# Performance work log

Measured on AMD Instinct MI355X. Metric: run time of the kernel, lower is better.

The kernel has to match this reference:

```python
import jax, jax.numpy as jnp
import numpy as np
import math

B, S, D, H = 64, 512, 768, 12
HS = D // H  # head size = 64


def setup_inputs() -> dict:
    key = jax.random.key(0)
    ks = jax.random.split(key, 8)
    scale = 1.0 / math.sqrt(D)
    return {
        "from_tensor": jax.random.normal(ks[0], (B, S, D), jnp.float32),
        "to_tensor": jax.random.normal(ks[1], (B, S, D), jnp.float32),
        "Wq": jax.random.normal(ks[2], (D, D), jnp.float32) * scale,
        "bq": jax.random.normal(ks[3], (D,), jnp.float32) * 0.02,
        "Wk": jax.random.normal(ks[4], (D, D), jnp.float32) * scale,
        "bk": jax.random.normal(ks[5], (D,), jnp.float32) * 0.02,
        "Wv": jax.random.normal(ks[6], (D, D), jnp.float32) * scale,
        "bv": jax.random.normal(ks[7], (D,), jnp.float32) * 0.02,
    }


def _split_heads(x):
    # [B, S, D] -> [B, H, S, HS]
    return x.reshape(B, S, H, HS).transpose(0, 2, 1, 3)


def reference(from_tensor, to_tensor, Wq, bq, Wk, bk, Wv, bv):
    q = _split_heads(from_tensor @ Wq + bq)
    k = _split_heads(to_tensor @ Wk + bk)
    v = _split_heads(to_tensor @ Wv + bv)
    scores = jnp.einsum("bhqd,bhkd->bhqk", q, k) / math.sqrt(HS)
    probs = jax.nn.softmax(scores, axis=-1)
    out = jnp.einsum("bhqk,bhkd->bhqd", probs, v)
    return out.transpose(0, 2, 1, 3).reshape(B, S, D)
```

## Files before the change

kernel.cpp:

```cpp
#include <hip/hip_runtime.h>
#include <hip/hip_bf16.h>

#define GAS __attribute__((address_space(1)))
#define LAS __attribute__((address_space(3)))

typedef __attribute__((ext_vector_type(8))) short   bf16x8;
typedef __attribute__((ext_vector_type(4))) float   f32x4;
typedef __attribute__((ext_vector_type(16))) float  f32x16;
typedef __attribute__((ext_vector_type(4))) float   f4;
typedef __attribute__((ext_vector_type(8))) short   s8v;
typedef __attribute__((ext_vector_type(2))) unsigned int u32x2;
typedef __attribute__((ext_vector_type(4))) unsigned int u32x4;

#define NB  64
#define NS  512
#define ND  768
#define NH  12
#define NHS 64
#define NM  (NB*NS)
#define NBH (NB*NH)

#define QSCALE 0.18033688011112042f

__device__ __forceinline__ unsigned short f2bf(float x){
  unsigned int u = __float_as_uint(x);
  u += 0x7fffu + ((u >> 16) & 1u);
  return (unsigned short)(u >> 16);
}

__device__ __forceinline__ f32x4 mfma16(bf16x8 a, bf16x8 b, f32x4 c){
  return __builtin_amdgcn_mfma_f32_16x16x32_bf16(a, b, c, 0, 0, 0);
}

__device__ __forceinline__ f32x16 mfma32(bf16x8 a, bf16x8 b, f32x16 c){
  return __builtin_amdgcn_mfma_f32_32x32x16_bf16(a, b, c, 0, 0, 0);
}

__device__ __forceinline__ unsigned int cvtpk(float lo, float hi){
  unsigned int r;
  asm("v_cvt_pk_bf16_f32 %0, %1, %2" : "=v"(r) : "v"(lo), "v"(hi));
  return r;
}

__device__ __forceinline__ bf16x8 u2b(u32x4 u){
  union { u32x4 a; bf16x8 b; } c; c.a = u; return c.b;
}

__global__ void cvt_w(const float* __restrict__ Wq, const float* __restrict__ Wk,
                      const float* __restrict__ Wv, short* __restrict__ Wt){
  int i = blockIdx.x * 256 + threadIdx.x;
  int mat = i / (ND*ND);
  int rem = i - mat * (ND*ND);
  int k = rem / ND;
  int n = rem - k * ND;
  const float* W = (mat == 0) ? Wq : (mat == 1 ? Wk : Wv);
  Wt[(long)mat*ND*ND + (long)n*ND + k] = (short)f2bf(W[rem]);
}

__global__ __launch_bounds__(512, 2)
void qkv_gemm(const float* __restrict__ from_t, const float* __restrict__ to_t,
              const short* __restrict__ Wt,
              const float* __restrict__ bq, const float* __restrict__ bk,
              const float* __restrict__ bv,
              short* __restrict__ Qw, short* __restrict__ Kw, short* __restrict__ Vtw){
  __shared__ short smem[65536];

  int bid = blockIdx.x;
  int wg  = (bid & 7) * 144 + (bid >> 3);
  int mat = wg / 384;
  int r   = wg - mat * 384;
  int mt  = r / 3;
  int nt  = r - mt * 3;

  const float* Af = (mat == 0) ? from_t : to_t;
  const short* Wp = Wt + (long)mat * ND * ND;

  int t_ = threadIdx.x, wv = t_ >> 6, l = t_ & 63, g = l >> 4, c = l & 15;
  int wm = wv >> 2, wn = wv & 3;
  int m0 = mt * 256, n0 = nt * 256;

  f4 areg[4];

  auto stageA_load = [&](int kt2){
    #pragma unroll
    for (int j = 0; j < 2; ++j){
      int idx = j * 512 + t_;
      int row = idx >> 2, slot = idx & 3;
      const float* gp = Af + (long)(m0 + row) * ND + kt2 * 32 + slot * 8;
      areg[j * 2]     = *(const f4*)(gp);
      areg[j * 2 + 1] = *(const f4*)(gp + 4);
    }
  };
  auto stageA_write = [&](int kt2){
    short* base = smem + (kt2 & 3) * 8192;
    #pragma unroll
    for (int j = 0; j < 2; ++j){
      int idx = j * 512 + t_;
      int row = idx >> 2, slot = idx & 3;
      int sw = slot ^ ((row >> 1) & 3);
      u32x4 pk;
      pk[0] = cvtpk(areg[j * 2][0],     areg[j * 2][1]);
      pk[1] = cvtpk(areg[j * 2][2],     areg[j * 2][3]);
      pk[2] = cvtpk(areg[j * 2 + 1][0], areg[j * 2 + 1][1]);
      pk[3] = cvtpk(areg[j * 2 + 1][2], areg[j * 2 + 1][3]);
      *(bf16x8*)(base + row * 32 + sw * 8) = u2b(pk);
    }
  };
  auto stageB = [&](int kt2){
    short* base = smem + 32768 + (kt2 & 3) * 8192;
    #pragma unroll
    for (int j = 0; j < 2; ++j){
      int idx = j * 512 + t_;
      int row = idx >> 2, slot = idx & 3;
      const short* gp = Wp + (long)(n0 + row) * ND + kt2 * 32 + ((slot ^ ((row >> 1) & 3)) << 3);
      __builtin_amdgcn_global_load_lds((const GAS unsigned int*)gp,
                                       (LAS unsigned int*)(base + idx * 8), 16, 0, 0);
    }
  };

  f32x4 zero = {0.f, 0.f, 0.f, 0.f};
  f32x4 acc[8][4];
  #pragma unroll
  for (int i = 0; i < 8; ++i)
    #pragma unroll
    for (int j = 0; j < 4; ++j) acc[i][j] = zero;

  stageB(0);
  stageA_load(0);
  stageA_write(0);
  stageA_load(1);
  stageA_write(1);
  stageA_load(2);
  stageB(1); stageB(2);
  asm volatile("s_waitcnt vmcnt(8)" ::: "memory");
  asm volatile("s_waitcnt lgkmcnt(0)" ::: "memory");
  __builtin_amdgcn_s_barrier();

  bf16x8 bfr[4];
  for (int kt = 0; kt < 24; ++kt){
    int sl = kt & 3;
    const short* Asl = smem + sl * 8192;
    const short* Bsl = smem + 32768 + sl * 8192;

    bf16x8 af[4];
    #pragma unroll
    for (int i = 0; i < 4; ++i){
      int row = wm * 128 + i * 16 + c;
      af[i] = *(const bf16x8*)(Asl + row * 32 + ((g ^ ((row >> 1) & 3)) << 3));
    }
    #pragma unroll
    for (int ns = 0; ns < 4; ++ns){
      int row = wn * 64 + ns * 16 + c;
      bfr[ns] = *(const bf16x8*)(Bsl + row * 32 + ((g ^ ((row >> 1) & 3)) << 3));
    }
    if (kt < 22) stageA_write(kt + 2);
    if (kt < 21) stageA_load(kt + 3);
    __builtin_amdgcn_s_barrier();
    asm volatile("s_waitcnt lgkmcnt(0)" ::: "memory");
    __builtin_amdgcn_sched_barrier(0);
    __builtin_amdgcn_s_setprio(1);
    #pragma unroll
    for (int i = 0; i < 4; ++i)
      #pragma unroll
      for (int ns = 0; ns < 4; ++ns)
        acc[i][ns] = mfma16(af[i], bfr[ns], acc[i][ns]);
    __builtin_amdgcn_s_setprio(0);
    __builtin_amdgcn_s_barrier();

    #pragma unroll
    for (int i = 0; i < 4; ++i){
      int row = wm * 128 + (4 + i) * 16 + c;
      af[i] = *(const bf16x8*)(Asl + row * 32 + ((g ^ ((row >> 1) & 3)) << 3));
    }
    if (kt < 21) stageB(kt + 3);
    __builtin_amdgcn_s_barrier();
    asm volatile("s_waitcnt lgkmcnt(0)" ::: "memory");
    __builtin_amdgcn_sched_barrier(0);
    __builtin_amdgcn_s_setprio(1);
    #pragma unroll
    for (int i = 0; i < 4; ++i)
      #pragma unroll
      for (int ns = 0; ns < 4; ++ns)
        acc[4 + i][ns] = mfma16(af[i], bfr[ns], acc[4 + i][ns]);
    __builtin_amdgcn_s_setprio(0);
    if (kt <= 20)      asm volatile("s_waitcnt vmcnt(8)" ::: "memory");
    else if (kt == 21) asm volatile("s_waitcnt vmcnt(2)" ::: "memory");
    else if (kt == 22) asm volatile("s_waitcnt vmcnt(0)" ::: "memory");
    __builtin_amdgcn_s_barrier();
  }

  int n0g = n0 + wn * 64;
  const float* bias = (mat == 0) ? bq : (mat == 1 ? bk : bv);
  float bb[4];
  #pragma unroll
  for (int ns = 0; ns < 4; ++ns) bb[ns] = bias[n0g + ns * 16 + c];
  short* chunk = smem + wv * 4096;
  int hq = n0g >> 6;

  if (mat < 2){
    short* O = (mat == 0) ? Qw : Kw;
    float scl = (mat == 0) ? QSCALE : 1.0f;
    #pragma unroll
    for (int sp = 0; sp < 2; ++sp){
      #pragma unroll
      for (int msl = 0; msl < 4; ++msl){
        #pragma unroll
        for (int ns = 0; ns < 4; ++ns){
          int col = ns * 16 + c;
          #pragma unroll
          for (int i = 0; i < 4; ++i){
            int row = msl * 16 + g * 4 + i;
            chunk[row * 64 + (((col >> 3) ^ (row & 7)) << 3) + (col & 7)] =
                (short)f2bf((acc[sp * 4 + msl][ns][i] + bb[ns]) * scl);
          }
        }
      }
      asm volatile("s_waitcnt lgkmcnt(0)" ::: "memory");
      __builtin_amdgcn_sched_barrier(0);
      #pragma unroll
      for (int rr = 0; rr < 8; ++rr){
        int row = rr * 8 + (l >> 3);
        int slot = l & 7;
        bf16x8 v = *(const bf16x8*)(chunk + row * 64 + ((slot ^ (row & 7)) << 3));
        int m = m0 + wm * 128 + sp * 64 + row;
        int b = m >> 9, s2 = m & 511;
        *(bf16x8*)(O + (((long)(b * NH + hq) * NS + s2) << 6) + slot * 8) = v;
      }
      if (sp == 0){ asm volatile("s_waitcnt lgkmcnt(0)" ::: "memory"); }
    }
  } else {
    #pragma unroll
    for (int sp = 0; sp < 2; ++sp){
      #pragma unroll
      for (int msl = 0; msl < 4; ++msl){
        #pragma unroll
        for (int ns = 0; ns < 4; ++ns){
          int hs = ns * 16 + c;
          #pragma unroll
          for (int i = 0; i < 4; ++i){
            int col = msl * 16 + g * 4 + i;
            chunk[hs * 64 + (((col >> 3) ^ (hs & 7)) << 3) + (col & 7)] =
                (short)f2bf(acc[sp * 4 + msl][ns][i] + bb[ns]);
          }
        }
      }
      asm volatile("s_waitcnt lgkmcnt(0)" ::: "memory");
      __builtin_amdgcn_sched_barrier(0);
      int mbase = m0 + wm * 128 + sp * 64;
      int b = mbase >> 9, s0 = mbase & 511;
      #pragma unroll
      for (int rr = 0; rr < 8; ++rr){
        int hs = rr * 8 + (l >> 3);
        int slot = l & 7;
        bf16x8 v = *(const bf16x8*)(chunk + hs * 64 + ((slot ^ (hs & 7)) << 3));
        *(bf16x8*)(Vtw + (long)((b * NH + hq) * 64 + hs) * NS + s0 + slot * 8) = v;
      }
      if (sp == 0){ asm volatile("s_waitcnt lgkmcnt(0)" ::: "memory"); }
    }
  }
}

__global__ __launch_bounds__(512, 1)
void attn_kernel(const short* __restrict__ Qw, const short* __restrict__ Kw,
                 const short* __restrict__ Vtw, float* __restrict__ out){
  extern __shared__ char smem[];
  short* Ks = (short*)smem;
  short* Vs = (short*)(smem + 65536);

  int bh = blockIdx.x;
  int t = threadIdx.x, wv = t >> 6, l = t & 63;
  int lam = l & 31, hi = l >> 5;
  int r7 = lam & 7;

  const short* Kb = Kw  + (long)bh * NS * NHS;
  const short* Vb = Vtw + (long)bh * NS * NHS;

  #pragma unroll
  for (int it = 0; it < 8; ++it){
    int chunk = it * 8 + wv;
    {
      int idx = chunk * 64 + l;
      int row = idx >> 3, slot = idx & 7;
      const short* gk = Kb + row * 64 + ((slot ^ (row & 7)) * 8);
      __builtin_amdgcn_global_load_lds((const GAS unsigned int*)gk,
                                       (LAS unsigned int*)(Ks + chunk * 512), 16, 0, 0);
    }
    {
      int row = chunk, slot = l;
      const short* gv = Vb + (long)row * NS + (((slot & 56) | ((slot & 7) ^ (row & 7))) * 8);
      __builtin_amdgcn_global_load_lds((const GAS unsigned int*)gv,
                                       (LAS unsigned int*)(Vs + chunk * 512), 16, 0, 0);
    }
  }
  __syncthreads();

  int b = bh / NH, h = bh - b * NH;
  float* outb = out + (long)b * NS * ND + (long)h * 64;

  for (int qt = 0; qt < 2; ++qt){
    int q0 = wv * 64 + qt * 32;
    const short* Qb = Qw + (((long)bh * NS + q0 + lam) << 6) + hi * 8;
    bf16x8 qf[4];
    #pragma unroll
    for (int dk = 0; dk < 4; ++dk) qf[dk] = *(const bf16x8*)(Qb + dk * 16);

    f32x16 o0, o1;
    #pragma unroll
    for (int j = 0; j < 16; ++j){ o0[j] = 0.f; o1[j] = 0.f; }
    float m_run = -1e30f, lsum = 0.f;

    #pragma unroll
    for (int ch = 0; ch < 16; ++ch){
      f32x16 s;
      #pragma unroll
      for (int j = 0; j < 16; ++j) s[j] = 0.f;
      const char* kbase = (const char*)Ks + (ch * 32 + lam) * 128;
      #pragma unroll
      for (int dk = 0; dk < 4; ++dk){
        bf16x8 kf = *(const bf16x8*)(kbase + (((hi + 2 * dk) ^ r7) << 4));
        s = mfma32(kf, qf[dk], s);
      }

      float t8[8], t4[4];
      #pragma unroll
      for (int j = 0; j < 8; ++j) t8[j] = fmaxf(s[j], s[j + 8]);
      #pragma unroll
      for (int j = 0; j < 4; ++j) t4[j] = fmaxf(t8[j], t8[j + 4]);
      float m1 = fmaxf(fmaxf(t4[0], t4[1]), fmaxf(t4[2], t4[3]));
      float pmax = fmaxf(m1, __shfl_xor(m1, 32));
      if (__any(pmax > m_run + 8.0f)){
        float mnew = fmaxf(m_run, pmax);
        float cf = exp2f(m_run - mnew);
        lsum *= cf;
        #pragma unroll
        for (int j = 0; j < 16; ++j){ o0[j] *= cf; o1[j] *= cf; }
        m_run = mnew;
      }
      float p[16];
      #pragma unroll
      for (int j = 0; j < 16; ++j) p[j] = exp2f(s[j] - m_run);
      float a8[8], a4[4];
      #pragma unroll
      for (int j = 0; j < 8; ++j) a8[j] = p[j] + p[j + 8];
      #pragma unroll
      for (int j = 0; j < 4; ++j) a4[j] = a8[j] + a8[j + 4];
      lsum += (a4[0] + a4[1]) + (a4[2] + a4[3]);

      unsigned int w[8];
      #pragma unroll
      for (int rr = 0; rr < 8; ++rr) w[rr] = cvtpk(p[2 * rr], p[2 * rr + 1]);
      unsigned int y0 = (unsigned int)__shfl_xor((int)(hi ? w[0] : w[2]), 32);
      unsigned int y1 = (unsigned int)__shfl_xor((int)(hi ? w[1] : w[3]), 32);
      unsigned int y2 = (unsigned int)__shfl_xor((int)(hi ? w[4] : w[6]), 32);
      unsigned int y3 = (unsigned int)__shfl_xor((int)(hi ? w[5] : w[7]), 32);
      u32x4 fa, fb;
      if (hi){
        fa[0] = y0;   fa[1] = y1;   fa[2] = w[2]; fa[3] = w[3];
        fb[0] = y2;   fb[1] = y3;   fb[2] = w[6]; fb[3] = w[7];
      } else {
        fa[0] = w[0]; fa[1] = w[1]; fa[2] = y0;   fa[3] = y1;
        fb[0] = w[4]; fb[1] = w[5]; fb[2] = y2;   fb[3] = y3;
      }
      bf16x8 pa = u2b(fa), pb = u2b(fb);

      const char* vb0 = (const char*)Vs + lam * 1024;
      const char* vb1 = (const char*)Vs + (32 + lam) * 1024;
      int sl0 = ch * 4 + hi, sl1 = ch * 4 + 2 + hi;
      int sw0 = ((sl0 & 56) | ((sl0 & 7) ^ r7)) << 4;
      int sw1 = ((sl1 & 56) | ((sl1 & 7) ^ r7)) << 4;
      bf16x8 v00 = *(const bf16x8*)(vb0 + sw0);
      bf16x8 v01 = *(const bf16x8*)(vb0 + sw1);
      bf16x8 v10 = *(const bf16x8*)(vb1 + sw0);
      bf16x8 v11 = *(const bf16x8*)(vb1 + sw1);
      o0 = mfma32(v00, pa, o0);
      o0 = mfma32(v01, pb, o0);
      o1 = mfma32(v10, pa, o1);
      o1 = mfma32(v11, pb, o1);
    }

    float lt = lsum + __shfl_xor(lsum, 32);
    float invl = 1.0f / lt;
    float* orow = outb + (long)(q0 + lam) * ND;
    #pragma unroll
    for (int r = 0; r < 4; ++r){
      f4 u0, u1;
      #pragma unroll
      for (int jj = 0; jj < 4; ++jj){
        u0[jj] = o0[4 * r + jj] * invl;
        u1[jj] = o1[4 * r + jj] * invl;
      }
      *(f4*)(orow + 4 * hi + 8 * r)      = u0;
      *(f4*)(orow + 32 + 4 * hi + 8 * r) = u1;
    }
  }
}

extern "C" void kernel_launch(void* const* d_in, const int* in_sizes, int n_in,
                              void* d_out, int out_size, void* d_ws, size_t ws_size,
                              hipStream_t stream){
  const float* from_t = (const float*)d_in[0];
  const float* to_t   = (const float*)d_in[1];
  const float* Wq = (const float*)d_in[2];
  const float* bq = (const float*)d_in[3];
  const float* Wk = (const float*)d_in[4];
  const float* bk = (const float*)d_in[5];
  const float* Wv = (const float*)d_in[6];
  const float* bv = (const float*)d_in[7];

  short* Wt  = (short*)d_ws;
  short* Qw  = Wt  + 1769472;
  short* Kw  = Qw  + 25165824;
  short* Vtw = Kw  + 25165824;

  cvt_w<<<6912, 256, 0, stream>>>(Wq, Wk, Wv, Wt);
  qkv_gemm<<<1152, 512, 0, stream>>>(from_t, to_t, Wt, bq, bk, bv, Qw, Kw, Vtw);
  attn_kernel<<<768, 512, 131072, stream>>>(Qw, Kw, Vtw, (float*)d_out);
}
```

Baseline: 312.2 us.

## Software-pipeline QK^T MFMA one chunk ahead of softmax with setprio hints

Restructures the attention inner loop so the QK^T MFMAs for the next key chunk are issued while the current chunk's softmax exp/max work runs. The next chunk's K fragments are prefetched from LDS into a double-buffered register array. s_setprio raises wave priority around MFMA bursts to encourage overlap across waves. This costs extra VGPRs for the second score accumulator and K fragments, which may lower occupancy or cause spills.

```diff
diff --git a/kernel.cpp b/kernel.cpp
--- a/kernel.cpp
+++ b/kernel.cpp
@@ -9,7 +9,6 @@
 typedef __attribute__((ext_vector_type(16))) float  f32x16;
 typedef __attribute__((ext_vector_type(4))) float   f4;
 typedef __attribute__((ext_vector_type(8))) short   s8v;
-typedef __attribute__((ext_vector_type(2))) unsigned int u32x2;
 typedef __attribute__((ext_vector_type(4))) unsigned int u32x4;
 
 #define NB  64
@@ -18,7 +17,6 @@
 #define NH  12
 #define NHS 64
 #define NM  (NB*NS)
-#define NBH (NB*NH)
 
 #define QSCALE 0.18033688011112042f
 
@@ -309,21 +307,35 @@
     for (int j = 0; j < 16; ++j){ o0[j] = 0.f; o1[j] = 0.f; }
     float m_run = -1e30f, lsum = 0.f;
 
+    f32x16 s2[2];
+    bf16x8 kfr[2][4];
+    {
+      const char* kb = (const char*)Ks + lam * 128;
+      #pragma unroll
+      for (int dk = 0; dk < 4; ++dk)
+        kfr[0][dk] = *(const bf16x8*)(kb + (((hi + 2 * dk) ^ r7) << 4));
+      #pragma unroll
+      for (int j = 0; j < 16; ++j) s2[0][j] = 0.f;
+      __builtin_amdgcn_s_setprio(1);
+      #pragma unroll
+      for (int dk = 0; dk < 4; ++dk) s2[0] = mfma32(kfr[0][dk], qf[dk], s2[0]);
+      __builtin_amdgcn_s_setprio(0);
+    }
+
     #pragma unroll
     for (int ch = 0; ch < 16; ++ch){
-      f32x16 s;
-      #pragma unroll
-      for (int j = 0; j < 16; ++j) s[j] = 0.f;
-      const char* kbase = (const char*)Ks + (ch * 32 + lam) * 128;
-      #pragma unroll
-      for (int dk = 0; dk < 4; ++dk){
-        bf16x8 kf = *(const bf16x8*)(kbase + (((hi + 2 * dk) ^ r7) << 4));
-        s = mfma32(kf, qf[dk], s);
+      const int cur = ch & 1, nxt = cur ^ 1;
+
+      if (ch < 15){
+        const char* kb = (const char*)Ks + ((ch + 1) * 32 + lam) * 128;
+        #pragma unroll
+        for (int dk = 0; dk < 4; ++dk)
+          kfr[nxt][dk] = *(const bf16x8*)(kb + (((hi + 2 * dk) ^ r7) << 4));
       }
 
       float t8[8], t4[4];
       #pragma unroll
-      for (int j = 0; j < 8; ++j) t8[j] = fmaxf(s[j], s[j + 8]);
+      for (int j = 0; j < 8; ++j) t8[j] = fmaxf(s2[cur][j], s2[cur][j + 8]);
       #pragma unroll
       for (int j = 0; j < 4; ++j) t4[j] = fmaxf(t8[j], t8[j + 4]);
       float m1 = fmaxf(fmaxf(t4[0], t4[1]), fmaxf(t4[2], t4[3]));
@@ -338,13 +350,22 @@
       }
       float p[16];
       #pragma unroll
-      for (int j = 0; j < 16; ++j) p[j] = exp2f(s[j] - m_run);
+      for (int j = 0; j < 16; ++j) p[j] = exp2f(s2[cur][j] - m_run);
       float a8[8], a4[4];
       #pragma unroll
       for (int j = 0; j < 8; ++j) a8[j] = p[j] + p[j + 8];
       #pragma unroll
       for (int j = 0; j < 4; ++j) a4[j] = a8[j] + a8[j + 4];
       lsum += (a4[0] + a4[1]) + (a4[2] + a4[3]);
+
+      if (ch < 15){
+        #pragma unroll
+        for (int j = 0; j < 16; ++j) s2[nxt][j] = 0.f;
+        __builtin_amdgcn_s_setprio(1);
+        #pragma unroll
+        for (int dk = 0; dk < 4; ++dk) s2[nxt] = mfma32(kfr[nxt][dk], qf[dk], s2[nxt]);
+        __builtin_amdgcn_s_setprio(0);
+      }
 
       unsigned int w[8];
       #pragma unroll
@@ -372,10 +393,12 @@
       bf16x8 v01 = *(const bf16x8*)(vb0 + sw1);
       bf16x8 v10 = *(const bf16x8*)(vb1 + sw0);
       bf16x8 v11 = *(const bf16x8*)(vb1 + sw1);
+      __builtin_amdgcn_s_setprio(1);
       o0 = mfma32(v00, pa, o0);
       o0 = mfma32(v01, pb, o0);
       o1 = mfma32(v10, pa, o1);
       o1 = mfma32(v11, pb, o1);
+      __builtin_amdgcn_s_setprio(0);
     }
 
     float lt = lsum + __shfl_xor(lsum, 32);
```

New measurement: 307.0 us. Within noise of the previous version (-1.7%).
